# Performance work log

Hardware: AMD Instinct MI355X
Metric: run time of the kernel (lower is better)

The kernel has to match this reference:

```python
import jax, jax.numpy as jnp
import numpy as np
from jax import lax

K_DIM, E_DIM, H_DIM, BETA = 256, 64, 256, 0.25
DN = ('NCHW', 'OIHW', 'NCHW')


def conv(x, w, b=None, stride=1, pad=0):
    y = lax.conv_general_dilated(x, w, (stride, stride), [(pad, pad), (pad, pad)], dimension_numbers=DN)
    if b is not None:
        y = y + b[None, :, None, None]
    return y


def deconv(x, w, b):
    # torch ConvTranspose2d(k=4, stride=2, pad=1): weight [in, out, kH, kW]
    rhs = jnp.flip(w, (2, 3)).swapaxes(0, 1)  # -> [out, in, kH, kW]
    y = lax.conv_general_dilated(x, rhs, (1, 1), [(2, 2), (2, 2)], lhs_dilation=(2, 2), dimension_numbers=DN)
    return y + b[None, :, None, None]


def res_block(x, w3, w1):
    out = jax.nn.relu(x)
    out = conv(out, w3, stride=1, pad=1)
    out = jax.nn.relu(out)
    out = conv(out, w1, stride=1, pad=0)
    return out + x


def vq_embed(z, codebook):
    # z: [B, C, Hs, Ws]; faithful to original: flatten to (-1, e_dim) even though C != e_dim
    zp = jnp.transpose(z, (0, 2, 3, 1))  # [B,Hs,Ws,C]
    zf = zp.reshape(-1, E_DIM)  # [N, e_dim]
    # ||z||^2 + ||e||^2 - 2 z e^T
    dist = (jnp.sum(zf * zf, axis=1, keepdims=True)
            + jnp.sum(codebook * codebook, axis=1)
            - 2.0 * zf @ codebook.T)  # [N, K]
    idx = jnp.argmin(dist, axis=1)  # [N]
    vq = jnp.take(codebook, idx, axis=0).reshape(zp.shape)  # gather == one-hot matmul
    loss = (jnp.mean((lax.stop_gradient(vq) - zp) ** 2)
            + BETA * jnp.mean((vq - lax.stop_gradient(zp)) ** 2))
    vq_st = zp + lax.stop_gradient(vq - zp)  # straight-through
    return loss, jnp.transpose(vq_st, (0, 3, 1, 2))


def setup_inputs() -> dict:
    key = jax.random.key(0)
    ks = jax.random.split(key, 20)
    f32 = jnp.float32
    s = 0.05
    inp = {
        'x': jax.random.normal(ks[0], (32, 3, 128, 128), f32),
        'enc_w1': jax.random.normal(ks[1], (H_DIM, 3, 4, 4), f32) * s,
        'enc_b1': jnp.zeros((H_DIM,), f32),
        'enc_w2': jax.random.normal(ks[2], (H_DIM, H_DIM, 4, 4), f32) * s,
        'enc_b2': jnp.zeros((H_DIM,), f32),
        'er1_w3': jax.random.normal(ks[3], (H_DIM, H_DIM, 3, 3), f32) * s,
        'er1_w1': jax.random.normal(ks[4], (H_DIM, H_DIM, 1, 1), f32) * s,
        'er2_w3': jax.random.normal(ks[5], (H_DIM, H_DIM, 3, 3), f32) * s,
        'er2_w1': jax.random.normal(ks[6], (H_DIM, H_DIM, 1, 1), f32) * s,
        'codebook': jax.random.uniform(ks[7], (K_DIM, E_DIM), f32, -1.0 / K_DIM, 1.0 / K_DIM),
        'dr1_w3': jax.random.normal(ks[8], (H_DIM, H_DIM, 3, 3), f32) * s,
        'dr1_w1': jax.random.normal(ks[9], (H_DIM, H_DIM, 1, 1), f32) * s,
        'dr2_w3': jax.random.normal(ks[10], (H_DIM, H_DIM, 3, 3), f32) * s,
        'dr2_w1': jax.random.normal(ks[11], (H_DIM, H_DIM, 1, 1), f32) * s,
        'dt1_w': jax.random.normal(ks[12], (H_DIM, H_DIM, 4, 4), f32) * s,  # [in,out,k,k]
        'dt1_b': jnp.zeros((H_DIM,), f32),
        'dt2_w': jax.random.normal(ks[13], (H_DIM, 3, 4, 4), f32) * s,
        'dt2_b': jnp.zeros((3,), f32),
    }
    return inp


def reference(x, enc_w1, enc_b1, enc_w2, enc_b2, er1_w3, er1_w1, er2_w3, er2_w1,
              codebook, dr1_w3, dr1_w1, dr2_w3, dr2_w1, dt1_w, dt1_b, dt2_w, dt2_b):
    # encoder
    z = conv(x, enc_w1, enc_b1, stride=2, pad=1)
    z = conv(z, enc_w2, enc_b2, stride=2, pad=1)
    z = res_block(z, er1_w3, er1_w1)
    z = res_block(z, er2_w3, er2_w1)
    # VQ
    emb_loss, vq_z = vq_embed(z, codebook)
    # decoder
    d = res_block(vq_z, dr1_w3, dr1_w1)
    d = res_block(d, dr2_w3, dr2_w1)
    d = deconv(d, dt1_w, dt1_b)
    d = deconv(d, dt2_w, dt2_b)
    recon = jnp.tanh(d)
    return recon, emb_loss
```

## Files before the change

### kernel.cpp

```cpp
#include <hip/hip_runtime.h>
#include <math.h>


typedef unsigned short ushort;
typedef short bf16x8 __attribute__((ext_vector_type(8)));
typedef float f32x4 __attribute__((ext_vector_type(4)));

__device__ __forceinline__ ushort f2bf(float f) {
    unsigned u = __builtin_bit_cast(unsigned, f);
    unsigned r = (u + 0x7fffu + ((u >> 16) & 1u)) >> 16;
    return (ushort)r;
}
__device__ __forceinline__ float bfl(unsigned u) { return __builtin_bit_cast(float, u << 16); }
__device__ __forceinline__ float bfh(unsigned u) { return __builtin_bit_cast(float, u & 0xffff0000u); }

__device__ __forceinline__ unsigned relu_u(unsigned u) {
    unsigned m = (u >> 15) & 0x00010001u;
    return u & ~((m << 16) - m);
}
__device__ __forceinline__ uint4 relu4(uint4 v) {
    v.x = relu_u(v.x); v.y = relu_u(v.y); v.z = relu_u(v.z); v.w = relu_u(v.w);
    return v;
}

__global__ void k_pack_c3x4(const float* __restrict__ w0, const float* __restrict__ w1,
                            const float* __restrict__ w2, const float* __restrict__ w3,
                            ushort* __restrict__ o0, ushort* __restrict__ o1,
                            ushort* __restrict__ o2, ushort* __restrict__ o3) {
    int layer = blockIdx.x / 2304;
    int i = (blockIdx.x - layer * 2304) * 256 + threadIdx.x;
    const float* w = layer == 0 ? w0 : layer == 1 ? w1 : layer == 2 ? w2 : w3;
    ushort* o = layer == 0 ? o0 : layer == 1 ? o1 : layer == 2 ? o2 : o3;
    int kk = i & 31, co = (i >> 5) & 255, cb = (i >> 13) & 7, t = i >> 16;
    int ci = cb * 32 + kk, kh = t / 3, kw = t % 3;
    o[i] = f2bf(w[((co * 256 + ci) * 3 + kh) * 3 + kw]);
}

__global__ void k_pack_c1x1x4(const float* __restrict__ w0, const float* __restrict__ w1,
                              const float* __restrict__ w2, const float* __restrict__ w3,
                              ushort* __restrict__ o0, ushort* __restrict__ o1,
                              ushort* __restrict__ o2, ushort* __restrict__ o3) {
    int layer = blockIdx.x >> 8;
    int i = (blockIdx.x & 255) * 256 + threadIdx.x;
    const float* w = layer == 0 ? w0 : layer == 1 ? w1 : layer == 2 ? w2 : w3;
    ushort* o = layer == 0 ? o0 : layer == 1 ? o1 : layer == 2 ? o2 : o3;
    int kk = i & 31, co = (i >> 5) & 255, cb = (i >> 13) & 7;
    o[i] = f2bf(w[co * 256 + cb * 32 + kk]);
}

__global__ void k_pack_vq(const float* __restrict__ cb, ushort* __restrict__ apk,
                          float* __restrict__ en) {
    if (blockIdx.x < 64) {
        int i = blockIdx.x * 256 + threadIdx.x;
        int j = i & 7, lane = (i >> 3) & 63, s = (i >> 9) & 1, t = i >> 10;
        int code = t * 16 + (lane & 15);
        int dim = s * 32 + (lane >> 4) * 8 + j;
        apk[i] = f2bf(cb[code * 64 + dim]);
    } else {
        int code = threadIdx.x;
        float s = 0.f;
        for (int d = 0; d < 64; ++d) { float v = cb[code * 64 + d]; s += v * v; }
        en[code] = s;
    }
}

__global__ __launch_bounds__(256) void k_wcomp_enc(const float* __restrict__ w1,
                                                   const float* __restrict__ b1f,
                                                   const float* __restrict__ w2,
                                                   const float* __restrict__ b2f,
                                                   ushort* __restrict__ wenc,
                                                   float* __restrict__ benc,
                                                   float* __restrict__ wct,
                                                   float* __restrict__ wcb,
                                                   float* __restrict__ wcl,
                                                   float* __restrict__ wcr,
                                                   float* __restrict__ wcc) {
    __shared__ float sw1[12288];
    __shared__ float sw2[4096];
    __shared__ float part[2400];
    int co = blockIdx.x, tid = threadIdx.x;
    for (int i = tid; i < 12288; i += 256) sw1[i] = w1[i];
    for (int i = tid; i < 4096; i += 256) sw2[i] = w2[co * 4096 + i];
    __syncthreads();

    {
        float s = 0.f;
#pragma unroll
        for (int t = 0; t < 16; ++t) s += sw2[tid * 16 + t];
        float pb = b1f[tid] * s;
#pragma unroll
        for (int m = 1; m < 64; m <<= 1) pb += __shfl_xor(pb, m);
        if ((tid & 63) == 0) part[tid >> 6] = pb;
    }
    __syncthreads();
    if (tid == 0) benc[co] = b2f[co] + part[0] + part[1] + part[2] + part[3];

    if (tid < 240) {
        int y = tid / 24, rem = tid % 24, ci = rem / 8, ms = rem % 8;
        int na = 0, aa[2], h1[2];
#pragma unroll
        for (int a = 0; a < 4; ++a) {
            int k1 = y - 2 * a;
            if ((unsigned)k1 < 4u) { aa[na] = a; h1[na] = k1; ++na; }
        }
        float acc10[10];
#pragma unroll
        for (int xx = 0; xx < 10; ++xx) acc10[xx] = 0.f;
        for (int m = ms * 32; m < ms * 32 + 32; ++m) {
            for (int pa = 0; pa < na; ++pa) {
                float4 a2 = *(const float4*)&sw2[m * 16 + aa[pa] * 4];
                float4 a1 = *(const float4*)&sw1[m * 48 + ci * 16 + h1[pa] * 4];
                acc10[0] += a2.x * a1.x; acc10[1] += a2.x * a1.y; acc10[2] += a2.x * a1.z; acc10[3] += a2.x * a1.w;
                acc10[2] += a2.y * a1.x; acc10[3] += a2.y * a1.y; acc10[4] += a2.y * a1.z; acc10[5] += a2.y * a1.w;
                acc10[4] += a2.z * a1.x; acc10[5] += a2.z * a1.y; acc10[6] += a2.z * a1.z; acc10[7] += a2.z * a1.w;
                acc10[6] += a2.w * a1.x; acc10[7] += a2.w * a1.y; acc10[8] += a2.w * a1.z; acc10[9] += a2.w * a1.w;
            }
        }
#pragma unroll
        for (int xx = 0; xx < 10; ++xx) part[tid * 10 + xx] = acc10[xx];
    }
    __syncthreads();
    for (int w = tid; w < 320; w += 256) {
        if (w < 300) {
            int y = w / 30, r = w % 30, ci = r / 10, xx = r % 10;
            float s = 0.f;
#pragma unroll
            for (int ms = 0; ms < 8; ++ms) s += part[((y * 24 + ci * 8) + ms) * 10 + xx];
            wenc[(y * 256 + co) * 32 + xx * 3 + ci] = f2bf(s);
        } else {
            int j = w - 300;
            int y = j >> 1;
            wenc[(y * 256 + co) * 32 + 30 + (j & 1)] = 0;
        }
    }

    if (tid < 30 || (tid >= 32 && tid < 62)) {
        bool top = tid < 30;
        int t = top ? tid : tid - 32;
        int xx = t / 3, ci = t % 3;
        int k2hf = top ? 0 : 3, k1hf = top ? 3 : 0;
        float s = 0.f;
        for (int m = 0; m < 256; ++m)
            for (int k2w = 0; k2w < 4; ++k2w) {
                int k1w = xx - 2 * k2w;
                if ((unsigned)k1w < 4u)
                    s += sw2[m * 16 + k2hf * 4 + k2w] * sw1[m * 48 + ci * 16 + k1hf * 4 + k1w];
            }
        (top ? wct : wcb)[t * 256 + co] = s;
    } else if ((tid >= 64 && tid < 94) || (tid >= 96 && tid < 126)) {
        bool left = tid < 94;
        int t = left ? tid - 64 : tid - 96;
        int y = t / 3, ci = t % 3;
        int k2wf = left ? 0 : 3, k1wf = left ? 3 : 0;
        float s = 0.f;
        for (int m = 0; m < 256; ++m)
            for (int k2h = 0; k2h < 4; ++k2h) {
                int k1h = y - 2 * k2h;
                if ((unsigned)k1h < 4u)
                    s += sw2[m * 16 + k2h * 4 + k2wf] * sw1[m * 48 + ci * 16 + k1h * 4 + k1wf];
            }
        (left ? wcl : wcr)[t * 256 + co] = s;
    } else if (tid >= 128 && tid < 140) {
        int c = (tid - 128) / 3, ci = (tid - 128) % 3;
        int k2h = (c >> 1) ? 3 : 0, k2w = (c & 1) ? 3 : 0;
        int k1h = 3 - k2h, k1w = 3 - k2w;
        float s = 0.f;
        for (int m = 0; m < 256; ++m)
            s += sw2[m * 16 + k2h * 4 + k2w] * sw1[m * 48 + ci * 16 + k1h * 4 + k1w];
        wcc[(c * 3 + ci) * 256 + co] = s;
    }
}

__global__ __launch_bounds__(256) void k_wcomp_dec(const float* __restrict__ dt1,
                                                   const float* __restrict__ dt1b,
                                                   const float* __restrict__ dt2,
                                                   const float* __restrict__ dt2b,
                                                   ushort* __restrict__ wdec,
                                                   float* __restrict__ bdec) {
    __shared__ float s1[4096];
    __shared__ float s2[12288];
    __shared__ float part[2400];
    int ci = blockIdx.x, tid = threadIdx.x;
    for (int i = tid; i < 4096; i += 256) s1[i] = dt1[ci * 4096 + i];
    for (int i = tid; i < 12288; i += 256) s2[i] = dt2[i];
    __syncthreads();

    if (ci == 0 && tid < 48) {
        int o = tid >> 4, p = tid & 15, py = p >> 2, px = p & 3;
        int c0 = (py + 1) & 1, d0 = (px + 1) & 1;
        float s = dt2b[o];
        for (int m = 0; m < 256; ++m) {
            float t2 = s2[m * 48 + o * 16 + c0 * 4 + d0] + s2[m * 48 + o * 16 + c0 * 4 + d0 + 2]
                     + s2[m * 48 + o * 16 + (c0 + 2) * 4 + d0] + s2[m * 48 + o * 16 + (c0 + 2) * 4 + d0 + 2];
            s += dt1b[m] * t2;
        }
        bdec[tid] = s;
    }

    if (tid < 240) {
        int y = tid / 24, rem = tid % 24, o = rem / 8, ms = rem % 8;
        int na = 0, aa[2], cc[2];
#pragma unroll
        for (int a = 0; a < 4; ++a) {
            int c = y - 2 * a;
            if ((unsigned)c < 4u) { aa[na] = a; cc[na] = c; ++na; }
        }
        float acc10[10];
#pragma unroll
        for (int xx = 0; xx < 10; ++xx) acc10[xx] = 0.f;
        for (int m = ms * 32; m < ms * 32 + 32; ++m) {
            for (int pa = 0; pa < na; ++pa) {
                float4 d1 = *(const float4*)&s1[m * 16 + aa[pa] * 4];
                float4 d2 = *(const float4*)&s2[m * 48 + o * 16 + cc[pa] * 4];
                acc10[0] += d1.x * d2.x; acc10[1] += d1.x * d2.y; acc10[2] += d1.x * d2.z; acc10[3] += d1.x * d2.w;
                acc10[2] += d1.y * d2.x; acc10[3] += d1.y * d2.y; acc10[4] += d1.y * d2.z; acc10[5] += d1.y * d2.w;
                acc10[4] += d1.z * d2.x; acc10[5] += d1.z * d2.y; acc10[6] += d1.z * d2.z; acc10[7] += d1.z * d2.w;
                acc10[6] += d1.w * d2.x; acc10[7] += d1.w * d2.y; acc10[8] += d1.w * d2.z; acc10[9] += d1.w * d2.w;
            }
        }
#pragma unroll
        for (int xx = 0; xx < 10; ++xx) part[tid * 10 + xx] = acc10[xx];
    }
    __syncthreads();
    for (int w = tid; w < 300; w += 256) {
        int y = w / 30, r = w % 30, o = r / 10, xx = r % 10;
        float s = 0.f;
#pragma unroll
        for (int ms = 0; ms < 8; ++ms) s += part[((y * 24 + o * 8) + ms) * 10 + xx];
        int du = (y < 3) ? 1 : (y < 7) ? 0 : -1;
        int py = y - 3 + 4 * du;
        int dv = (xx < 3) ? 1 : (xx < 7) ? 0 : -1;
        int px = xx - 3 + 4 * dv;
        int t = (du + 1) * 3 + (dv + 1);
        int cb2 = ci >> 5, kk = ci & 31;
        wdec[((((t * 3 + o) * 8 + cb2) * 16 + py * 4 + px) * 32) + kk] = f2bf(s);
    }
}

__global__ void k_xpack(const float* __restrict__ x, ushort* __restrict__ xpk) {
    int i = blockIdx.x * 256 + threadIdx.x;
    int j = i & 7, ow = (i >> 3) & 31, q = (i >> 8) & 3, r = (i >> 10) & 127, n = i >> 17;
    int k = q * 8 + j;
    float v = 0.f;
    if (k < 30) {
        int ci = k % 3, kw = k / 3;
        int col = 4 * ow - 3 + kw;
        if ((unsigned)col < 128u) v = x[((n * 3 + ci) * 128 + r) * 128 + col];
    }
    xpk[i] = f2bf(v);
}

__global__ __launch_bounds__(128) void k_enc_comp(const ushort* __restrict__ xpk,
                                                  const ushort* __restrict__ wenc,
                                                  const float* __restrict__ benc,
                                                  ushort* __restrict__ obf) {
    int tid = threadIdx.x, lane = tid & 63, wv = tid >> 6;
    int q = lane >> 4, l15 = lane & 15;
    int b = blockIdx.x;
    int mblk = b & 7, coslab = (b >> 3) & 3, n = b >> 5;
    int R0 = mblk * 4 + wv * 2;
    int aoff = (coslab * 64 + l15) * 32 + q * 8;

    f32x4 acc[4][4];
#pragma unroll
    for (int at = 0; at < 4; ++at)
#pragma unroll
        for (int bt = 0; bt < 4; ++bt) acc[at][bt] = 0.f;

    for (int t = 0; t < 10; ++t) {
        bf16x8 af[4];
#pragma unroll
        for (int at = 0; at < 4; ++at)
            af[at] = *(const bf16x8*)(wenc + t * 8192 + aoff + at * 512);
#pragma unroll
        for (int bt2 = 0; bt2 < 2; ++bt2) {
            int irow = 4 * (R0 + bt2) + t - 3;
            if ((unsigned)irow >= 128u) continue;
            bf16x8 bf[2];
#pragma unroll
            for (int hb = 0; hb < 2; ++hb) {
                int ow = hb * 16 + l15;
                bf[hb] = *(const bf16x8*)(xpk + ((((long)n * 128 + irow) * 4 + q) * 32 + ow) * 8);
            }
#pragma unroll
            for (int at = 0; at < 4; ++at)
#pragma unroll
                for (int hb = 0; hb < 2; ++hb)
                    acc[at][bt2 * 2 + hb] = __builtin_amdgcn_mfma_f32_16x16x32_bf16(
                        af[at], bf[hb], acc[at][bt2 * 2 + hb], 0, 0, 0);
        }
    }

    int co_base = coslab * 64;
#pragma unroll
    for (int at = 0; at < 4; ++at) {
        int co_t = co_base + at * 16 + q * 4;
        float4 b4 = *(const float4*)(benc + co_t);
        float bv[4] = {b4.x, b4.y, b4.z, b4.w};
#pragma unroll
        for (int bt = 0; bt < 4; ++bt) {
            int m = R0 * 32 + bt * 16 + l15;
            long oaddr = ((long)n * 1024 + m) * 256 + co_t;
            float v[4];
#pragma unroll
            for (int r = 0; r < 4; ++r) v[r] = acc[at][bt][r] + bv[r];
            uint2 pk;
            pk.x = (unsigned)f2bf(v[0]) | ((unsigned)f2bf(v[1]) << 16);
            pk.y = (unsigned)f2bf(v[2]) | ((unsigned)f2bf(v[3]) << 16);
            *(uint2*)(obf + oaddr) = pk;
        }
    }
}

__global__ __launch_bounds__(256) void k_fix_border(const float* __restrict__ x,
                                                    const ushort* __restrict__ xpk,
                                                    const float* __restrict__ wct,
                                                    const float* __restrict__ wcb,
                                                    const float* __restrict__ wcl,
                                                    const float* __restrict__ wcr,
                                                    const float* __restrict__ wcc,
                                                    ushort* __restrict__ X0) {
    int b = blockIdx.x;
    int n = b >> 7, job = b & 127;
    if (job >= 124) return;
    int co = threadIdx.x;

    auto dot_tb = [&](const float* __restrict__ w, int row, int qq) -> float {
        const ushort* xr = xpk + ((long)n * 128 + row) * 1024;
        float s = 0.f;
        for (int k = 0; k < 30; ++k)
            s += w[k * 256 + co] * bfl((unsigned)xr[(k >> 3) * 256 + qq * 8 + (k & 7)]);
        return s;
    };
    auto dot_lr = [&](const float* __restrict__ w, int p, int colofs) -> float {
        float s = 0.f;
        for (int y = 0; y < 10; ++y) {
            int row = 4 * p - 3 + y;
            if ((unsigned)row >= 128u) continue;
            for (int ci = 0; ci < 3; ++ci)
                s += w[(y * 3 + ci) * 256 + co] * x[((long)(n * 3 + ci) * 128 + row) * 128 + colofs];
        }
        return s;
    };
    auto corner = [&](int c, int row, int colofs) -> float {
        float s = 0.f;
        for (int ci = 0; ci < 3; ++ci)
            s += wcc[(c * 3 + ci) * 256 + co] * x[((long)(n * 3 + ci) * 128 + row) * 128 + colofs];
        return s;
    };

    int m;
    float corr;
    if (job < 32) {
        int qq = job;
        m = qq;
        corr = dot_tb(wct, 0, qq);
        if (qq == 0)  corr += dot_lr(wcl, 0, 0)   - corner(0, 0, 0);
        if (qq == 31) corr += dot_lr(wcr, 0, 127) - corner(1, 0, 127);
    } else if (job < 64) {
        int qq = job - 32;
        m = 992 + qq;
        corr = dot_tb(wcb, 127, qq);
        if (qq == 0)  corr += dot_lr(wcl, 31, 0)   - corner(2, 127, 0);
        if (qq == 31) corr += dot_lr(wcr, 31, 127) - corner(3, 127, 127);
    } else if (job < 94) {
        int p = job - 63;
        m = 32 * p;
        corr = dot_lr(wcl, p, 0);
    } else {
        int p = job - 93;
        m = 32 * p + 31;
        corr = dot_lr(wcr, p, 127);
    }

    ushort* ptr = X0 + ((long)n * 1024 + m) * 256 + co;
    float v = bfl((unsigned)(*ptr));
    *ptr = f2bf(v - corr);
}

__global__ __launch_bounds__(256, 2) void k_resblock(const ushort* __restrict__ xin,
                                                     const ushort* __restrict__ w3pk,
                                                     const ushort* __restrict__ w1pk,
                                                     ushort* __restrict__ obf) {
    constexpr int BUFU = 4 * 4 * 34 * 8;
    __shared__ __align__(16) ushort sX[2 * BUFU];
    __shared__ __align__(16) ushort sEx[64 * 256];

    int tid = threadIdx.x, lane = tid & 63, wv = tid >> 6;
    int q = lane >> 4, l15 = lane & 15;
    int b = blockIdx.x;
    int rp = b & 15, n = b >> 4;
    int R0 = rp * 2;

    if (tid < 64) {
        int bufi = tid >> 5, rq = (tid >> 1) & 15, cc = (tid & 1) ? 33 : 0;
        uint4 z; z.x = z.y = z.z = z.w = 0;
        *(uint4*)&sX[bufi * BUFU + (rq * 34 + cc) * 8] = z;
    }

    int brr[4], bcol[4];
#pragma unroll
    for (int bt = 0; bt < 4; ++bt) {
        int p = bt * 16 + l15;
        brr[bt] = p >> 5; bcol[bt] = (p & 31) + 1;
    }

    int scol = lane >> 1, j0 = (lane & 1) * 2;
    int aoff = (wv * 64 + l15) * 32 + q * 8;

    f32x4 acc[4][4];
#pragma unroll
    for (int at = 0; at < 4; ++at)
#pragma unroll
        for (int bt = 0; bt < 4; ++bt) acc[at][bt] = 0.f;

    int hh = R0 - 1 + wv;
    bool hvalid = (unsigned)hh < 32u;
    uint4 sreg[2];
    auto stage_load = [&](int cb2) {
        long off = (((long)n * 32 + hh) * 32 + scol) * 256 + cb2 * 32 + j0 * 8;
#pragma unroll
        for (int k = 0; k < 2; ++k) {
            uint4 v;
            if (hvalid) v = relu4(*(const uint4*)(xin + off + k * 8));
            else { v.x = 0; v.y = 0; v.z = 0; v.w = 0; }
            sreg[k] = v;
        }
    };
    auto write_stage = [&](int pbuf) {
        ushort* bufp = sX + pbuf * BUFU;
#pragma unroll
        for (int k = 0; k < 2; ++k)
            *(uint4*)&bufp[((wv * 4 + j0 + k) * 34 + scol + 1) * 8] = sreg[k];
    };

    stage_load(0);
    write_stage(0);

    bf16x8 afA[3][4];
    {
        const ushort* wb0 = w3pk + aoff;
#pragma unroll
        for (int at = 0; at < 4; ++at) afA[0][at] = *(const bf16x8*)(wb0 + at * 512);
#pragma unroll
        for (int at = 0; at < 4; ++at) afA[1][at] = *(const bf16x8*)(wb0 + 65536 + at * 512);
    }
    __syncthreads();

    for (int cb = 0; cb < 8; ++cb) {
        ushort* bufp = sX + (cb & 1) * BUFU;
        if (cb + 1 < 8) stage_load(cb + 1);
        const ushort* wb = w3pk + (long)cb * 8192 + aoff;
        const ushort* wbn = w3pk + (long)(cb + 1) * 8192 + aoff;

#pragma unroll
        for (int t = 0; t < 9; ++t) {
            if (t < 7) {
#pragma unroll
                for (int at = 0; at < 4; ++at)
                    afA[(t + 2) % 3][at] = *(const bf16x8*)(wb + (long)(t + 2) * 65536 + at * 512);
            } else if (cb < 7) {
#pragma unroll
                for (int at = 0; at < 4; ++at)
                    afA[(t + 2) % 3][at] = *(const bf16x8*)(wbn + (long)(t - 7) * 65536 + at * 512);
            }
            int taprow = t / 3, dx = t % 3 - 1;
            bf16x8 bfr[4];
#pragma unroll
            for (int bt = 0; bt < 4; ++bt)
                bfr[bt] = *(const bf16x8*)&bufp[(((brr[bt] + taprow) * 4 + q) * 34 + bcol[bt] + dx) * 8];
#pragma unroll
            for (int at = 0; at < 4; ++at)
#pragma unroll
                for (int bt = 0; bt < 4; ++bt)
                    acc[at][bt] = __builtin_amdgcn_mfma_f32_16x16x32_bf16(afA[t % 3][at], bfr[bt],
                                                                          acc[at][bt], 0, 0, 0);
        }

        if (cb + 1 < 8) {
            write_stage((cb + 1) & 1);
            __syncthreads();
        }
    }

#pragma unroll
    for (int at = 0; at < 4; ++at) {
        int co_t = wv * 64 + at * 16 + q * 4;
#pragma unroll
        for (int bt = 0; bt < 4; ++bt) {
            int px = bt * 16 + l15;
            uint2 pk;
            pk.x = (unsigned)f2bf(fmaxf(acc[at][bt][0], 0.f))
                 | ((unsigned)f2bf(fmaxf(acc[at][bt][1], 0.f)) << 16);
            pk.y = (unsigned)f2bf(fmaxf(acc[at][bt][2], 0.f))
                 | ((unsigned)f2bf(fmaxf(acc[at][bt][3], 0.f)) << 16);
            *(uint2*)&sEx[px * 256 + (co_t ^ ((px & 7) << 3))] = pk;
        }
    }
    __syncthreads();

    f32x4 acc2[4][4];
#pragma unroll
    for (int at = 0; at < 4; ++at)
#pragma unroll
        for (int bt = 0; bt < 4; ++bt) acc2[at][bt] = 0.f;

    bf16x8 af1c[4], af1n[4];
#pragma unroll
    for (int at = 0; at < 4; ++at) af1c[at] = *(const bf16x8*)(w1pk + aoff + at * 512);

    for (int cb = 0; cb < 8; ++cb) {
        if (cb + 1 < 8) {
            const ushort* wb1n = w1pk + (long)(cb + 1) * 8192 + aoff;
#pragma unroll
            for (int at = 0; at < 4; ++at) af1n[at] = *(const bf16x8*)(wb1n + at * 512);
        }
        bf16x8 bf1[4];
#pragma unroll
        for (int bt = 0; bt < 4; ++bt) {
            int px = bt * 16 + l15;
            bf1[bt] = *(const bf16x8*)&sEx[px * 256 + ((cb * 32 + q * 8) ^ ((px & 7) << 3))];
        }
#pragma unroll
        for (int at = 0; at < 4; ++at)
#pragma unroll
            for (int bt = 0; bt < 4; ++bt)
                acc2[at][bt] = __builtin_amdgcn_mfma_f32_16x16x32_bf16(af1c[at], bf1[bt],
                                                                      acc2[at][bt], 0, 0, 0);
        if (cb + 1 < 8) {
#pragma unroll
            for (int at = 0; at < 4; ++at) af1c[at] = af1n[at];
        }
    }

#pragma unroll
    for (int at = 0; at < 4; ++at) {
        int co_t = wv * 64 + at * 16 + q * 4;
#pragma unroll
        for (int bt = 0; bt < 4; ++bt) {
            int m = R0 * 32 + bt * 16 + l15;
            long oaddr = ((long)n * 1024 + m) * 256 + co_t;
            uint2 rr = *(const uint2*)(xin + oaddr);
            float v[4];
            v[0] = acc2[at][bt][0] + bfl(rr.x);
            v[1] = acc2[at][bt][1] + bfh(rr.x);
            v[2] = acc2[at][bt][2] + bfl(rr.y);
            v[3] = acc2[at][bt][3] + bfh(rr.y);
            uint2 pk;
            pk.x = (unsigned)f2bf(v[0]) | ((unsigned)f2bf(v[1]) << 16);
            pk.y = (unsigned)f2bf(v[2]) | ((unsigned)f2bf(v[3]) << 16);
            *(uint2*)(obf + oaddr) = pk;
        }
    }
}

__global__ __launch_bounds__(256) void k_vq2(const ushort* __restrict__ zb,
                                             const ushort* __restrict__ apk,
                                             const float* __restrict__ en,
                                             const float* __restrict__ cbf,
                                             ushort* __restrict__ vqb,
                                             float* __restrict__ loss) {
    __shared__ int sIdx[64];
    __shared__ float sLoss[64];
    int tid = threadIdx.x, lane = tid & 63, wv = tid >> 6;
    int q = lane >> 4, l15 = lane & 15;
    int r0 = blockIdx.x * 64;
    int R = r0 + wv * 16;

    const ushort* zp = zb + ((long)(R + l15)) * 64 + q * 8;
    bf16x8 b0 = *(const bf16x8*)zp;
    bf16x8 b1 = *(const bf16x8*)(zp + 32);

    float z2 = 0.f;
    {
        const unsigned* u0 = (const unsigned*)&b0;
        const unsigned* u1 = (const unsigned*)&b1;
#pragma unroll
        for (int i = 0; i < 4; ++i) {
            float a = bfl(u0[i]), bb = bfh(u0[i]);
            float c = bfl(u1[i]), d = bfh(u1[i]);
            z2 += a * a + bb * bb + c * c + d * d;
        }
    }

    float best = 3.4e38f;
    int bidx = 0;
#pragma unroll
    for (int t = 0; t < 16; ++t) {
        bf16x8 a0 = *(const bf16x8*)(apk + ((t * 2 + 0) * 64 + lane) * 8);
        bf16x8 a1 = *(const bf16x8*)(apk + ((t * 2 + 1) * 64 + lane) * 8);
        f32x4 acc = {0.f, 0.f, 0.f, 0.f};
        acc = __builtin_amdgcn_mfma_f32_16x16x32_bf16(a0, b0, acc, 0, 0, 0);
        acc = __builtin_amdgcn_mfma_f32_16x16x32_bf16(a1, b1, acc, 0, 0, 0);
        float4 e4 = *(const float4*)(en + t * 16 + q * 4);
        float sc[4] = {e4.x - 2.f * acc[0], e4.y - 2.f * acc[1],
                       e4.z - 2.f * acc[2], e4.w - 2.f * acc[3]};
#pragma unroll
        for (int r = 0; r < 4; ++r) {
            int code = t * 16 + q * 4 + r;
            if (sc[r] < best) { best = sc[r]; bidx = code; }
        }
    }
#pragma unroll
    for (int m = 16; m <= 32; m <<= 1) {
        float ob = __shfl_xor(best, m);
        int oi = __shfl_xor(bidx, m);
        if (ob < best || (ob == best && oi < bidx)) { best = ob; bidx = oi; }
        z2 += __shfl_xor(z2, m);
    }
    if (q == 0) {
        sIdx[wv * 16 + l15] = bidx;
        sLoss[wv * 16 + l15] = best + z2;
    }
    __syncthreads();

    if (wv == 0) {
        float l = sLoss[lane];
#pragma unroll
        for (int m = 1; m < 64; m <<= 1) l += __shfl_xor(l, m);
        if (lane == 0) atomicAdd(loss, l * (1.25f / 8388608.f));
    }

    unsigned* vb = (unsigned*)(vqb + (long)r0 * 64);
#pragma unroll
    for (int k = 0; k < 8; ++k) {
        int i = k * 256 + tid;
        int rl = i >> 5, jp = i & 31;
        int idx = sIdx[rl];
        float v0 = cbf[idx * 64 + 2 * jp];
        float v1 = cbf[idx * 64 + 2 * jp + 1];
        vb[i] = (unsigned)f2bf(v0) | ((unsigned)f2bf(v1) << 16);
    }
}

__global__ __launch_bounds__(128, 2) void k_dec_comp(const ushort* __restrict__ xin,
                                                     const ushort* __restrict__ wdec,
                                                     const float* __restrict__ bdec,
                                                     float* __restrict__ out) {
    constexpr int BUFU = 3 * 4 * 34 * 8;
    constexpr int WLDS = 2 * BUFU;
    __shared__ __align__(16) ushort sX[2 * WLDS];
    __shared__ __align__(16) float sOut[3072];

    int tid = threadIdx.x, lane = tid & 63, wv = tid >> 6;
    int q = lane >> 4, l15 = lane & 15;
    int b = blockIdx.x;
    int rp = b & 15, n = b >> 4;
    int U = rp * 2 + wv;
    ushort* sW = sX + wv * WLDS;

    if (lane < 48) {
        int cc = (lane & 1) ? 33 : 0;
        int sq = lane >> 1;
        uint4 z; z.x = z.y = z.z = z.w = 0;
        *(uint4*)&sW[(sq * 34 + cc) * 8] = z;
    }
    int scol = lane >> 1, j0 = (lane & 1) * 2;

    f32x4 acc[3][2];
#pragma unroll
    for (int o = 0; o < 3; ++o)
#pragma unroll
        for (int bt = 0; bt < 2; ++bt) acc[o][bt] = 0.f;

    uint4 sreg[3][2];
    auto stage_load = [&](int cb2) {
#pragma unroll
        for (int r = 0; r < 3; ++r) {
            int hh = U - 1 + r;
            bool valid = (unsigned)hh < 32u;
            long off = (((long)n * 32 + hh) * 32 + scol) * 256 + cb2 * 32 + j0 * 8;
#pragma unroll
            for (int k = 0; k < 2; ++k) {
                uint4 v;
                if (valid) v = *(const uint4*)(xin + off + k * 8);
                else { v.x = 0; v.y = 0; v.z = 0; v.w = 0; }
                sreg[r][k] = v;
            }
        }
    };
    auto write_stage = [&](int pbuf) {
        ushort* bufp = sW + pbuf * BUFU;
#pragma unroll
        for (int r = 0; r < 3; ++r)
#pragma unroll
            for (int k = 0; k < 2; ++k)
                *(uint4*)&bufp[((r * 4 + j0 + k) * 34 + scol + 1) * 8] = sreg[r][k];
    };

    stage_load(0);
    write_stage(0);

    for (int cb = 0; cb < 8; ++cb) {
        ushort* bufp = sW + (cb & 1) * BUFU;
        if (cb + 1 < 8) stage_load(cb + 1);
        const ushort* wb = wdec + (long)cb * 512 + l15 * 32 + q * 8;
#pragma unroll
        for (int t = 0; t < 9; ++t) {
            int du = t / 3 - 1, dv = t % 3 - 1;
            bf16x8 bfr[2];
#pragma unroll
            for (int bt = 0; bt < 2; ++bt)
                bfr[bt] = *(const bf16x8*)&bufp[(((du + 1) * 4 + q) * 34 + bt * 16 + l15 + 1 + dv) * 8];
#pragma unroll
            for (int o = 0; o < 3; ++o) {
                bf16x8 af = *(const bf16x8*)(wb + (long)(t * 3 + o) * 4096);
#pragma unroll
                for (int bt = 0; bt < 2; ++bt)
                    acc[o][bt] = __builtin_amdgcn_mfma_f32_16x16x32_bf16(af, bfr[bt], acc[o][bt], 0, 0, 0);
            }
        }
        if (cb + 1 < 8) write_stage((cb + 1) & 1);
    }

#pragma unroll
    for (int o = 0; o < 3; ++o) {
#pragma unroll
        for (int bt = 0; bt < 2; ++bt) {
            int V = bt * 16 + l15;
#pragma unroll
            for (int r = 0; r < 4; ++r) {
                int p = q * 4 + r, py = p >> 2, px = p & 3;
                sOut[((o * 2 + wv) * 4 + py) * 128 + 4 * V + px] =
                    tanhf(acc[o][bt][r] + bdec[o * 16 + p]);
            }
        }
    }
    __syncthreads();

#pragma unroll
    for (int i = 0; i < 6; ++i) {
        int idx = i * 128 + tid;
        int row = idx >> 5, colq = idx & 31;
        int o = row >> 3, rem = row & 7, wv2 = rem >> 2, py = rem & 3;
        long g = ((((long)n * 3 + o) * 128) + 4 * (rp * 2 + wv2) + py) * 128 + colq * 4;
        *(float4*)(out + g) = *(float4*)&sOut[row * 128 + colq * 4];
    }
}

extern "C" void kernel_launch(void* const* d_in, const int* in_sizes, int n_in,
                              void* d_out, int out_size, void* d_ws, size_t ws_size,
                              hipStream_t stream) {
    (void)in_sizes; (void)n_in; (void)out_size; (void)ws_size;
    const float* x        = (const float*)d_in[0];
    const float* enc_w1   = (const float*)d_in[1];
    const float* enc_b1   = (const float*)d_in[2];
    const float* enc_w2   = (const float*)d_in[3];
    const float* enc_b2   = (const float*)d_in[4];
    const float* er1_w3   = (const float*)d_in[5];
    const float* er1_w1   = (const float*)d_in[6];
    const float* er2_w3   = (const float*)d_in[7];
    const float* er2_w1   = (const float*)d_in[8];
    const float* codebook = (const float*)d_in[9];
    const float* dr1_w3   = (const float*)d_in[10];
    const float* dr1_w1   = (const float*)d_in[11];
    const float* dr2_w3   = (const float*)d_in[12];
    const float* dr2_w1   = (const float*)d_in[13];
    const float* dt1_w    = (const float*)d_in[14];
    const float* dt1_b    = (const float*)d_in[15];
    const float* dt2_w    = (const float*)d_in[16];
    const float* dt2_b    = (const float*)d_in[17];

    float* recon = (float*)d_out;
    float* loss  = recon + 1572864;

    char* ws = (char*)d_ws;
    size_t off = 0;
    auto alloc = [&](size_t bytes) { char* p = ws + off; off += (bytes + 255) & ~(size_t)255; return p; };
    ushort* X0   = (ushort*)alloc(16777216);
    ushort* X2   = (ushort*)alloc(16777216);
    ushort* X3   = (ushort*)alloc(16777216);
    ushort* X4   = (ushort*)alloc(16777216);
    ushort* xpk  = (ushort*)alloc(8388608);
    ushort* wpk_er13 = (ushort*)alloc(1179648);
    ushort* wpk_er23 = (ushort*)alloc(1179648);
    ushort* wpk_dr13 = (ushort*)alloc(1179648);
    ushort* wpk_dr23 = (ushort*)alloc(1179648);
    ushort* wpk_er11 = (ushort*)alloc(131072);
    ushort* wpk_er21 = (ushort*)alloc(131072);
    ushort* wpk_dr11 = (ushort*)alloc(131072);
    ushort* wpk_dr21 = (ushort*)alloc(131072);
    ushort* wenc     = (ushort*)alloc(163840);
    ushort* wdec     = (ushort*)alloc(221184);
    ushort* apk      = (ushort*)alloc(32768);
    float*  benc     = (float*)alloc(1024);
    float*  bdec     = (float*)alloc(192);
    float*  en       = (float*)alloc(1024);
    float*  wct      = (float*)alloc(32768);
    float*  wcb      = (float*)alloc(32768);
    float*  wcl      = (float*)alloc(32768);
    float*  wcr      = (float*)alloc(32768);
    float*  wcc      = (float*)alloc(12288);

    hipMemsetAsync(loss, 0, sizeof(float), stream);
    hipMemsetAsync(wdec, 0, 221184, stream);

    k_pack_c3x4<<<9216, 256, 0, stream>>>(er1_w3, er2_w3, dr1_w3, dr2_w3,
                                          wpk_er13, wpk_er23, wpk_dr13, wpk_dr23);
    k_pack_c1x1x4<<<1024, 256, 0, stream>>>(er1_w1, er2_w1, dr1_w1, dr2_w1,
                                            wpk_er11, wpk_er21, wpk_dr11, wpk_dr21);
    k_pack_vq<<<65, 256, 0, stream>>>(codebook, apk, en);
    k_wcomp_enc<<<256, 256, 0, stream>>>(enc_w1, enc_b1, enc_w2, enc_b2, wenc, benc,
                                         wct, wcb, wcl, wcr, wcc);
    k_wcomp_dec<<<256, 256, 0, stream>>>(dt1_w, dt1_b, dt2_w, dt2_b, wdec, bdec);
    k_xpack<<<16384, 256, 0, stream>>>(x, xpk);

    k_enc_comp<<<1024, 128, 0, stream>>>(xpk, wenc, benc, X0);
    k_fix_border<<<4096, 256, 0, stream>>>(x, xpk, wct, wcb, wcl, wcr, wcc, X0);
    k_resblock<<<512, 256, 0, stream>>>(X0, wpk_er13, wpk_er11, X2);
    k_resblock<<<512, 256, 0, stream>>>(X2, wpk_er23, wpk_er21, X3);
    k_vq2<<<2048, 256, 0, stream>>>(X3, apk, en, codebook, X4, loss);
    k_resblock<<<512, 256, 0, stream>>>(X4, wpk_dr13, wpk_dr11, X0);
    k_resblock<<<512, 256, 0, stream>>>(X0, wpk_dr23, wpk_dr21, X2);
    k_dec_comp<<<512, 128, 0, stream>>>(X2, wdec, bdec, recon);
}
```

Before: 534.1 us.

## Stage full input slab in LDS once, removing per-chunk double-buffer syncs

The residual-block kernel now loads all 256 channels of the 4-row input halo into one shared buffer up front, replacing the double-buffered per-channel-chunk staging with a barrier after each chunk. The same buffer is then reused for the intermediate activations of the 1x1 conv. This removes seven block-wide barriers and the register staging, but the global loads are no longer overlapped with the MFMA work. LDS use rises to about 70 KB per block, which may limit the two-blocks-per-CU occupancy target.

```diff
diff --git a/kernel.cpp b/kernel.cpp
--- a/kernel.cpp
+++ b/kernel.cpp
@@ -382,9 +382,7 @@
                                                      const ushort* __restrict__ w3pk,
                                                      const ushort* __restrict__ w1pk,
                                                      ushort* __restrict__ obf) {
-    constexpr int BUFU = 4 * 4 * 34 * 8;
-    __shared__ __align__(16) ushort sX[2 * BUFU];
-    __shared__ __align__(16) ushort sEx[64 * 256];
+    __shared__ __align__(16) ushort sS[4 * 32 * 34 * 8];
 
     int tid = threadIdx.x, lane = tid & 63, wv = tid >> 6;
     int q = lane >> 4, l15 = lane & 15;
@@ -392,50 +390,36 @@
     int rp = b & 15, n = b >> 4;
     int R0 = rp * 2;
 
-    if (tid < 64) {
-        int bufi = tid >> 5, rq = (tid >> 1) & 15, cc = (tid & 1) ? 33 : 0;
-        uint4 z; z.x = z.y = z.z = z.w = 0;
-        *(uint4*)&sX[bufi * BUFU + (rq * 34 + cc) * 8] = z;
-    }
-
     int brr[4], bcol[4];
 #pragma unroll
     for (int bt = 0; bt < 4; ++bt) {
         int p = bt * 16 + l15;
         brr[bt] = p >> 5; bcol[bt] = (p & 31) + 1;
     }
-
-    int scol = lane >> 1, j0 = (lane & 1) * 2;
     int aoff = (wv * 64 + l15) * 32 + q * 8;
 
+#pragma unroll
+    for (int it = 0; it < 16; ++it) {
+        int idx = it * 256 + tid;
+        int j = idx & 31, c = (idx >> 5) & 31, r = idx >> 10;
+        int hh2 = R0 - 1 + r;
+        uint4 v;
+        if ((unsigned)hh2 < 32u)
+            v = relu4(*(const uint4*)(xin + (((long)n * 32 + hh2) * 32 + c) * 256 + j * 8));
+        else { v.x = 0; v.y = 0; v.z = 0; v.w = 0; }
+        *(uint4*)&sS[((r * 32 + j) * 34 + c + 1) * 8] = v;
+    }
+    {
+        int r = tid >> 6, j = (tid >> 1) & 31, cc = (tid & 1) ? 33 : 0;
+        uint4 z; z.x = 0; z.y = 0; z.z = 0; z.w = 0;
+        *(uint4*)&sS[((r * 32 + j) * 34 + cc) * 8] = z;
+    }
+
     f32x4 acc[4][4];
 #pragma unroll
     for (int at = 0; at < 4; ++at)
 #pragma unroll
         for (int bt = 0; bt < 4; ++bt) acc[at][bt] = 0.f;
-
-    int hh = R0 - 1 + wv;
-    bool hvalid = (unsigned)hh < 32u;
-    uint4 sreg[2];
-    auto stage_load = [&](int cb2) {
-        long off = (((long)n * 32 + hh) * 32 + scol) * 256 + cb2 * 32 + j0 * 8;
-#pragma unroll
-        for (int k = 0; k < 2; ++k) {
-            uint4 v;
-            if (hvalid) v = relu4(*(const uint4*)(xin + off + k * 8));
-            else { v.x = 0; v.y = 0; v.z = 0; v.w = 0; }
-            sreg[k] = v;
-        }
-    };
-    auto write_stage = [&](int pbuf) {
-        ushort* bufp = sX + pbuf * BUFU;
-#pragma unroll
-        for (int k = 0; k < 2; ++k)
-            *(uint4*)&bufp[((wv * 4 + j0 + k) * 34 + scol + 1) * 8] = sreg[k];
-    };
-
-    stage_load(0);
-    write_stage(0);
 
     bf16x8 afA[3][4];
     {
@@ -448,10 +432,9 @@
     __syncthreads();
 
     for (int cb = 0; cb < 8; ++cb) {
-        ushort* bufp = sX + (cb & 1) * BUFU;
-        if (cb + 1 < 8) stage_load(cb + 1);
         const ushort* wb = w3pk + (long)cb * 8192 + aoff;
         const ushort* wbn = w3pk + (long)(cb + 1) * 8192 + aoff;
+        int qo = cb * 4 + q;
 
 #pragma unroll
         for (int t = 0; t < 9; ++t) {
@@ -468,7 +451,7 @@
             bf16x8 bfr[4];
 #pragma unroll
             for (int bt = 0; bt < 4; ++bt)
-                bfr[bt] = *(const bf16x8*)&bufp[(((brr[bt] + taprow) * 4 + q) * 34 + bcol[bt] + dx) * 8];
+                bfr[bt] = *(const bf16x8*)&sS[(((brr[bt] + taprow) * 32 + qo) * 34 + bcol[bt] + dx) * 8];
 #pragma unroll
             for (int at = 0; at < 4; ++at)
 #pragma unroll
@@ -476,12 +459,8 @@
                     acc[at][bt] = __builtin_amdgcn_mfma_f32_16x16x32_bf16(afA[t % 3][at], bfr[bt],
                                                                           acc[at][bt], 0, 0, 0);
         }
-
-        if (cb + 1 < 8) {
-            write_stage((cb + 1) & 1);
-            __syncthreads();
-        }
-    }
+    }
+    __syncthreads();
 
 #pragma unroll
     for (int at = 0; at < 4; ++at) {
@@ -494,7 +473,7 @@
                  | ((unsigned)f2bf(fmaxf(acc[at][bt][1], 0.f)) << 16);
             pk.y = (unsigned)f2bf(fmaxf(acc[at][bt][2], 0.f))
                  | ((unsigned)f2bf(fmaxf(acc[at][bt][3], 0.f)) << 16);
-            *(uint2*)&sEx[px * 256 + (co_t ^ ((px & 7) << 3))] = pk;
+            *(uint2*)&sS[px * 256 + (co_t ^ ((px & 7) << 3))] = pk;
         }
     }
     __syncthreads();
@@ -519,7 +498,7 @@
 #pragma unroll
         for (int bt = 0; bt < 4; ++bt) {
             int px = bt * 16 + l15;
-            bf1[bt] = *(const bf16x8*)&sEx[px * 256 + ((cb * 32 + q * 8) ^ ((px & 7) << 3))];
+            bf1[bt] = *(const bf16x8*)&sS[px * 256 + ((cb * 32 + q * 8) ^ ((px & 7) << 3))];
         }
 #pragma unroll
         for (int at = 0; at < 4; ++at)
```

Result: faster. 520.9 us (-2.5%).
